# Performance work log

Measured on AMD Instinct MI355X. Metric: run time of the kernel, lower is better.

The kernel has to match this reference:

```python
import jax, jax.numpy as jnp
import numpy as np

B, S, IN_DIM, D_MODEL, NUM_HEADS = 4, 2048, 1024, 1024, 16
HEAD_DIM = D_MODEL // NUM_HEADS
CAUSAL = True
NEG = -9000000000000000.0


def _xavier(key, shape):
    fan_out, fan_in = shape
    limit = (6.0 / (fan_in + fan_out)) ** 0.5
    return jax.random.uniform(key, shape, jnp.float32, -limit, limit)


def setup_inputs() -> dict:
    key = jax.random.key(0)
    ks = jax.random.split(key, 5)
    x = jax.random.normal(ks[0], (B, S, IN_DIM), jnp.float32)
    Wq = _xavier(ks[1], (D_MODEL, IN_DIM))
    Wk = _xavier(ks[2], (D_MODEL, IN_DIM))
    Wv = _xavier(ks[3], (D_MODEL, IN_DIM))
    Wo = _xavier(ks[4], (D_MODEL, D_MODEL))
    bq = jnp.zeros((D_MODEL,), jnp.float32)
    bk = jnp.zeros((D_MODEL,), jnp.float32)
    bv = jnp.zeros((D_MODEL,), jnp.float32)
    bo = jnp.zeros((D_MODEL,), jnp.float32)
    return {"x": x, "Wq": Wq, "bq": bq, "Wk": Wk, "bk": bk,
            "Wv": Wv, "bv": bv, "Wo": Wo, "bo": bo}


def reference(x, Wq, bq, Wk, bk, Wv, bv, Wo, bo):
    batch, seq, _ = x.shape
    # torch Linear: y = x @ W.T + b
    q = x @ Wq.T + bq
    k = x @ Wk.T + bk
    v = x @ Wv.T + bv
    # [B, S, H, Dh] -> [B, H, S, Dh]
    def split(t):
        return t.reshape(batch, seq, NUM_HEADS, HEAD_DIM).transpose(0, 2, 1, 3)
    q, k, v = split(q), split(k), split(v)
    scores = jnp.einsum('bhqd,bhkd->bhqk', q, k) / jnp.sqrt(jnp.float32(HEAD_DIM))
    if CAUSAL:
        mask = jnp.tril(jnp.ones((seq, seq), bool))
        scores = jnp.where(mask, scores, jnp.float32(NEG))
    attn = jax.nn.softmax(scores, axis=-1)
    out = jnp.einsum('bhqk,bhkd->bhqd', attn, v)
    out = out.transpose(0, 2, 1, 3).reshape(batch, seq, D_MODEL)
    return out @ Wo.T + bo
```

## Files before the change

kernel.cpp:

```cpp
#include <hip/hip_runtime.h>
#include <cstdint>
#include <cmath>

typedef unsigned short u16;
typedef __attribute__((ext_vector_type(4))) float f32x4;
typedef __attribute__((ext_vector_type(8))) short bf16x8;

#define D_MODEL 1024
#define SEQ     2048
#define BATCH   4
#define NHEAD   16
#define MTOT    (BATCH*SEQ)
#define NXE     ((size_t)MTOT * D_MODEL)

static_assert(sizeof(bf16x8) == 16, "frag size");

__device__ __forceinline__ float bf2f(u16 u) {
    union { uint32_t i; float f; } v; v.i = ((uint32_t)u) << 16; return v.f;
}
__device__ __forceinline__ u16 f2bf(float x) {
    union { float f; uint32_t i; } v; v.f = x;
    uint32_t r = (v.i + 0x7FFFu + ((v.i >> 16) & 1u)) >> 16;
    return (u16)r;
}
__device__ __forceinline__ u16 f2bf_trunc(float x) {
    union { float f; uint32_t i; } v; v.f = x;
    return (u16)(v.i >> 16);
}

#if defined(__has_builtin)
#if __has_builtin(__builtin_amdgcn_exp2f)
#define EXP2_FAST(x) __builtin_amdgcn_exp2f(x)
#endif
#endif
#ifndef EXP2_FAST
#define EXP2_FAST(x) exp2f(x)
#endif

typedef const __attribute__((address_space(1))) void* gptr_t;
typedef __attribute__((address_space(3))) void* sptr_t;
__device__ __forceinline__ void gload_lds16(const void* g, void* l) {
    __builtin_amdgcn_global_load_lds((gptr_t)g, (sptr_t)l, 16, 0, 0);
}

__device__ __forceinline__ u16 u4get(const uint4& v, int e) {
    const uint32_t w = ((e >> 1) == 0) ? v.x : ((e >> 1) == 1) ? v.y
                     : ((e >> 1) == 2) ? v.z : v.w;
    return (u16)((e & 1) ? (w >> 16) : (w & 0xFFFFu));
}

__global__ __launch_bounds__(256) void diag_write(float* __restrict__ out, float v) {
    size_t i = (size_t)blockIdx.x * 256 + threadIdx.x;
    for (; i < NXE; i += (size_t)gridDim.x * 256) out[i] = v;
}

__global__ void detect_dtype(const u16* __restrict__ x, int* __restrict__ flag) {
    __shared__ int cnt;
    if (threadIdx.x == 0) cnt = 0;
    __syncthreads();
    int c = 0;
#pragma unroll
    for (int k = 0; k < 16; ++k) {
        u16 e = x[2 * (threadIdx.x * 16 + k)];
        int ex = (e >> 7) & 0xFF;
        if (e == 0 || (ex >= 100 && ex <= 140)) ++c;
    }
    atomicAdd(&cnt, c);
    __syncthreads();
    if (threadIdx.x == 0) *flag = (cnt >= 3500) ? 1 : 0;
}

struct CvtArgs { const void* src[9]; u16* dst[9]; int n[9]; };

__global__ __launch_bounds__(256) void cvt_all(CvtArgs a, const int* __restrict__ flag) {
    const int seg = blockIdx.y;
    const int n = a.n[seg];
    const int i = (blockIdx.x * 256 + threadIdx.x) * 8;
    if (i >= n) return;
    u16* d = a.dst[seg] + i;
    if (*flag) {
        *(uint4*)d = *(const uint4*)((const u16*)a.src[seg] + i);
    } else {
        const float* s = (const float*)a.src[seg] + i;
        u16 tmp[8];
#pragma unroll
        for (int k = 0; k < 8; ++k) tmp[k] = f2bf(s[k]);
        *(uint4*)d = *(uint4*)tmp;
    }
}

template <typename OutT>
__device__ __forceinline__ void gemm_body(
    const u16* __restrict__ A, const u16* __restrict__ W,
    const u16* __restrict__ bias, OutT* __restrict__ C,
    int M, int N, int K)
{
    __shared__ __align__(16) u16 As[128 * 32];
    __shared__ __align__(16) u16 Bs[128 * 32];

    const int t    = threadIdx.x;
    const int wave = t >> 6;
    const int ln   = t & 15;
    const int qd   = (t >> 4) & 3;
    const int m0   = blockIdx.x * 128;
    const int n0   = blockIdx.y * 128;
    const int wm   = (wave >> 1) * 64;
    const int wn   = (wave & 1) * 64;

    const int srow = t >> 2;
    const int scol = (t & 3) * 8;
    const u16* gA = A + (size_t)(m0 + srow) * K + scol;
    const u16* gB = W + (size_t)(n0 + srow) * K + scol;
    u16* lA = &As[wave * 512];
    u16* lB = &Bs[wave * 512];

    f32x4 acc[4][4] = {};

    for (int k0 = 0; k0 < K; k0 += 32) {
        __syncthreads();
        gload_lds16(gA + k0,                   lA);
        gload_lds16(gA + (size_t)64 * K + k0,  lA + 2048);
        gload_lds16(gB + k0,                   lB);
        gload_lds16(gB + (size_t)64 * K + k0,  lB + 2048);
        __syncthreads();

        bf16x8 af[4], bfr[4];
#pragma unroll
        for (int i = 0; i < 4; ++i)
            af[i] = *(const bf16x8*)&As[(wm + i * 16 + ln) * 32 + qd * 8];
#pragma unroll
        for (int j = 0; j < 4; ++j)
            bfr[j] = *(const bf16x8*)&Bs[(wn + j * 16 + ln) * 32 + qd * 8];
#pragma unroll
        for (int i = 0; i < 4; ++i)
#pragma unroll
            for (int j = 0; j < 4; ++j)
                acc[i][j] = __builtin_amdgcn_mfma_f32_16x16x32_bf16(
                    af[i], bfr[j], acc[i][j], 0, 0, 0);
    }

    float bv[4];
#pragma unroll
    for (int j = 0; j < 4; ++j) bv[j] = bf2f(bias[n0 + wn + j * 16 + ln]);

#pragma unroll
    for (int i = 0; i < 4; ++i)
#pragma unroll
        for (int r = 0; r < 4; ++r) {
            int row = m0 + wm + i * 16 + qd * 4 + r;
            OutT* crow = C + (size_t)row * N + n0 + wn + ln;
#pragma unroll
            for (int j = 0; j < 4; ++j) {
                float v = acc[i][j][r] + bv[j];
                if constexpr (sizeof(OutT) == 2) crow[j * 16] = f2bf(v);
                else                             crow[j * 16] = v;
            }
        }
}

__global__ __launch_bounds__(256) void gemm_qkv(
    const u16* __restrict__ A,
    const u16* __restrict__ W0, const u16* __restrict__ W1, const u16* __restrict__ W2,
    const u16* __restrict__ b0, const u16* __restrict__ b1, const u16* __restrict__ b2,
    u16* __restrict__ C0, u16* __restrict__ C1, u16* __restrict__ C2,
    int M, int N, int K)
{
    const u16* W; const u16* bias; u16* C;
    if (blockIdx.z == 0)      { W = W0; bias = b0; C = C0; }
    else if (blockIdx.z == 1) { W = W1; bias = b1; C = C1; }
    else                      { W = W2; bias = b2; C = C2; }
    gemm_body<u16>(A, W, bias, C, M, N, K);
}

__global__ __launch_bounds__(256) void gemm_final_f32(
    const u16* __restrict__ A, const u16* __restrict__ W,
    const u16* __restrict__ bias, float* __restrict__ C, int M, int N, int K)
{
    gemm_body<float>(A, W, bias, C, M, N, K);
}

__global__ __launch_bounds__(256) void transpose_v(
    const u16* __restrict__ V, u16* __restrict__ VT)
{
    __shared__ u16 T[64][72];
    const int st = blockIdx.x;
    const int bh = blockIdx.y;
    const int b  = bh >> 4;
    const int h  = bh & 15;
    const int t  = threadIdx.x;

    const int sr = t >> 2;
    const int dc = (t & 3) * 16;
    const u16* src = V + ((size_t)b * SEQ + st * 64 + sr) * D_MODEL + h * 64 + dc;
    const uint4 a0 = *(const uint4*)src;
    const uint4 a1 = *(const uint4*)(src + 8);
#pragma unroll
    for (int e = 0; e < 8; ++e) T[dc + e][sr]     = u4get(a0, e);
#pragma unroll
    for (int e = 0; e < 8; ++e) T[dc + 8 + e][sr] = u4get(a1, e);
    __syncthreads();

    const int d  = t >> 2;
    const int sc = (t & 3) * 16;
    u16* dst = VT + ((size_t)bh * 64 + d) * SEQ + st * 64 + sc;
    *(uint4*)dst       = *(const uint4*)&T[d][sc];
    *(uint4*)(dst + 8) = *(const uint4*)&T[d][sc + 8];
}

__global__ __launch_bounds__(64) void flash_attn(
    const u16* __restrict__ Qg, const u16* __restrict__ Kg,
    const u16* __restrict__ VTg, u16* __restrict__ Og)
{
    __shared__ __align__(16) u16 Vsh[64 * 64];
    __shared__ __align__(16) u16 Psh[32 * 64];

    const int lane = threadIdx.x;
    const int ln   = lane & 15;
    const int qd   = lane >> 4;
    const int psw  = (ln & 7) << 3;

    const int bh = blockIdx.y;
    const int qw = (63 - (int)blockIdx.x + bh) & 63;
    const int b  = bh >> 4;
    const int h  = bh & 15;
    const int h0 = h * 64;
    const size_t rowBase = (size_t)b * SEQ * D_MODEL;
    const int qw0 = qw * 32;
    const int ktMax = qw >> 1;

    const int vdG = lane >> 3;
    const int vsw = ((lane & 7) * 8) ^ (vdG << 3);
    const u16* vtRow0 = VTg + ((size_t)(bh * 64 + vdG)) * SEQ + vsw;

    const float SCL = 0.18033688011112042f;

    bf16x8 qf[2][2];
#pragma unroll
    for (int i = 0; i < 2; ++i)
#pragma unroll
        for (int ks = 0; ks < 2; ++ks)
            qf[i][ks] = *(const bf16x8*)(Qg + rowBase
                + (size_t)(qw0 + i * 16 + ln) * D_MODEL + h0 + ks * 32 + qd * 8);

    float m_run[2], l_run[2];
#pragma unroll
    for (int i = 0; i < 2; ++i) { m_run[i] = -30000.0f; l_run[i] = 0.f; }
    f32x4 oacc[2][4] = {};

    for (int kt = 0; kt <= ktMax; ++kt) {
        __syncthreads();
        {
            const u16* vbase = vtRow0 + kt * 64;
#pragma unroll
            for (int p = 0; p < 8; ++p)
                gload_lds16(vbase + (size_t)(p * 8) * SEQ, &Vsh[p * 512]);
        }

        f32x4 sacc[4][2] = {};
#pragma unroll
        for (int ks = 0; ks < 2; ++ks) {
            bf16x8 kf[4];
#pragma unroll
            for (int j = 0; j < 4; ++j)
                kf[j] = *(const bf16x8*)(Kg + rowBase
                    + (size_t)(kt * 64 + j * 16 + ln) * D_MODEL + h0 + ks * 32 + qd * 8);
            __builtin_amdgcn_s_setprio(1);
#pragma unroll
            for (int j = 0; j < 4; ++j)
#pragma unroll
                for (int i = 0; i < 2; ++i)
                    sacc[j][i] = __builtin_amdgcn_mfma_f32_16x16x32_bf16(
                        kf[j], qf[i][ks], sacc[j][i], 0, 0, 0);
            __builtin_amdgcn_s_setprio(0);
        }

        if (kt == ktMax) {
#pragma unroll
            for (int j = 0; j < 4; ++j)
#pragma unroll
                for (int r = 0; r < 4; ++r) {
                    const int kpos = kt * 64 + j * 16 + qd * 4 + r;
#pragma unroll
                    for (int i = 0; i < 2; ++i) {
                        const int qpos = qw0 + i * 16 + ln;
                        float s = sacc[j][i][r] * SCL;
                        sacc[j][i][r] = (kpos > qpos) ? -30000.0f : s;
                    }
                }
        } else {
#pragma unroll
            for (int j = 0; j < 4; ++j)
#pragma unroll
                for (int i = 0; i < 2; ++i)
#pragma unroll
                    for (int r = 0; r < 4; ++r)
                        sacc[j][i][r] *= SCL;
        }

        float mx[2];
#pragma unroll
        for (int i = 0; i < 2; ++i) {
            float m0 = sacc[0][i][0];
#pragma unroll
            for (int j = 0; j < 4; ++j)
#pragma unroll
                for (int r = 0; r < 4; ++r) m0 = fmaxf(m0, sacc[j][i][r]);
            m0 = fmaxf(m0, __shfl_xor(m0, 16));
            m0 = fmaxf(m0, __shfl_xor(m0, 32));
            mx[i] = m0;
        }

        const bool grow = !(__all((mx[0] <= m_run[0] + 8.f) &&
                                  (mx[1] <= m_run[1] + 8.f)));
        if (grow) {
#pragma unroll
            for (int i = 0; i < 2; ++i) {
                const float mo = m_run[i];
                const float mn = fmaxf(mo, mx[i]);
                const float alpha = EXP2_FAST(mo - mn);
                m_run[i] = mn;
                l_run[i] *= alpha;
#pragma unroll
                for (int r = 0; r < 4; ++r) {
                    const float ar = __shfl(alpha, qd * 4 + r);
#pragma unroll
                    for (int j = 0; j < 4; ++j) oacc[i][j][r] *= ar;
                }
            }
        }

#pragma unroll
        for (int i = 0; i < 2; ++i) {
            const float mn = m_run[i];
            float rs = 0.f;
#pragma unroll
            for (int j = 0; j < 4; ++j) {
                u16 tp[4];
#pragma unroll
                for (int r = 0; r < 4; ++r) {
                    float p = EXP2_FAST(sacc[j][i][r] - mn);
                    rs += p;
                    tp[r] = f2bf_trunc(p);
                }
                uint2 w;
                w.x = (uint32_t)tp[0] | ((uint32_t)tp[1] << 16);
                w.y = (uint32_t)tp[2] | ((uint32_t)tp[3] << 16);
                *(uint2*)&Psh[(i * 16 + ln) * 64 + ((j * 16 + qd * 4) ^ psw)] = w;
            }
            rs += __shfl_xor(rs, 16);
            rs += __shfl_xor(rs, 32);
            l_run[i] += rs;
        }

        __syncthreads();

#pragma unroll
        for (int ks = 0; ks < 2; ++ks) {
            bf16x8 pa[2];
#pragma unroll
            for (int i = 0; i < 2; ++i)
                pa[i] = *(const bf16x8*)&Psh[(i * 16 + ln) * 64
                                             + ((ks * 32 + qd * 8) ^ psw)];
            __builtin_amdgcn_s_setprio(1);
#pragma unroll
            for (int j = 0; j < 4; ++j) {
                const int d = j * 16 + ln;
                const bf16x8 vb = *(const bf16x8*)&Vsh[d * 64
                    + ((ks * 32 + qd * 8) ^ ((ln & 7) << 3))];
#pragma unroll
                for (int i = 0; i < 2; ++i)
                    oacc[i][j] = __builtin_amdgcn_mfma_f32_16x16x32_bf16(
                        pa[i], vb, oacc[i][j], 0, 0, 0);
            }
            __builtin_amdgcn_s_setprio(0);
        }
    }

#pragma unroll
    for (int i = 0; i < 2; ++i)
#pragma unroll
        for (int r = 0; r < 4; ++r) {
            const float lr = __shfl(l_run[i], qd * 4 + r);
            const float inv = 1.f / lr;
            const int qrow = qw0 + i * 16 + qd * 4 + r;
            u16* orow = Og + rowBase + (size_t)qrow * D_MODEL + h0 + ln;
#pragma unroll
            for (int j = 0; j < 4; ++j)
                orow[j * 16] = f2bf(oacc[i][j][r] * inv);
        }
}

static inline bool ranges_overlap(const void* a, size_t an, const void* b, size_t bn) {
    uintptr_t x0 = (uintptr_t)a, x1 = x0 + an;
    uintptr_t y0 = (uintptr_t)b, y1 = y0 + bn;
    return x0 < y1 && y0 < x1;
}

extern "C" void kernel_launch(void* const* d_in, const int* in_sizes, int n_in,
                              void* d_out, int out_size, void* d_ws, size_t ws_size,
                              hipStream_t stream)
{
    int e = 0;
    const int expect[9] = { 8388608, 1048576, 1024, 1048576, 1024,
                            1048576, 1024, 1048576, 1024 };
    if (n_in != 9) e = 59;
    if (!e) for (int i = 0; i < 9; ++i)
        if (in_sizes[i] != expect[i]) { e = 60 + i; break; }
    if (!e && out_size != (int)NXE) e = 53;
    if (!e && ranges_overlap(d_ws, ws_size, d_out, (size_t)out_size * 4)) e = 55;

    const size_t NX = NXE;
    const size_t NW = (size_t)D_MODEL * D_MODEL;
    const size_t NB = D_MODEL;

    const size_t need = (64 + 4 * NW + 4 * NB + 2 * NX) * 2;
    if (!e && ws_size < need) e = 50;
    if (e) { diag_write<<<2048, 256, 0, stream>>>((float*)d_out, ldexpf(1.0f, e)); return; }

    u16* ws   = (u16*)d_ws;
    int* flag = (int*)ws;
    u16* Wqb  = ws + 64;
    u16* Wkb  = Wqb + NW;
    u16* Wvb  = Wkb + NW;
    u16* Wob  = Wvb + NW;
    u16* bqb  = Wob + NW;
    u16* bkb  = bqb + NB;
    u16* bvb  = bkb + NB;
    u16* bob  = bvb + NB;
    u16* Kw   = bob + NB;
    u16* Vw   = Kw  + NX;

    u16* xb  = (u16*)d_out;
    u16* Qw  = xb + NX;
    u16* VTw = xb;
    u16* Ow  = Vw;

    detect_dtype<<<1, 256, 0, stream>>>((const u16*)d_in[0], flag);

    CvtArgs ca;
    const void* srcs[9] = { d_in[0], d_in[1], d_in[3], d_in[5], d_in[7],
                            d_in[2], d_in[4], d_in[6], d_in[8] };
    u16* dsts[9] = { xb, Wqb, Wkb, Wvb, Wob, bqb, bkb, bvb, bob };
    int  ns[9]   = { (int)NX, (int)NW, (int)NW, (int)NW, (int)NW,
                     (int)NB, (int)NB, (int)NB, (int)NB };
    for (int i = 0; i < 9; ++i) { ca.src[i] = srcs[i]; ca.dst[i] = dsts[i]; ca.n[i] = ns[i]; }
    cvt_all<<<dim3((unsigned)((NX + 2047) / 2048), 9), 256, 0, stream>>>(ca, flag);

    gemm_qkv<<<dim3(MTOT / 128, D_MODEL / 128, 3), 256, 0, stream>>>(
        xb, Wqb, Wkb, Wvb, bqb, bkb, bvb, Qw, Kw, Vw, MTOT, D_MODEL, D_MODEL);

    transpose_v<<<dim3(SEQ / 64, BATCH * NHEAD), 256, 0, stream>>>(Vw, VTw);

    flash_attn<<<dim3(SEQ / 32, BATCH * NHEAD), 64, 0, stream>>>(Qw, Kw, VTw, Ow);

    gemm_final_f32<<<dim3(MTOT / 128, D_MODEL / 128), 256, 0, stream>>>(
        Ow, Wob, bob, (float*)d_out, MTOT, D_MODEL, D_MODEL);
}
```

Baseline: 334.2 us.

## Split flash-attention KV loop across two waves with final softmax merge

Each block now runs two waves that handle alternating key tiles for the same 32 query rows. Each wave keeps its own V and P shared-memory buffers, and the per-iteration __syncthreads become per-wave waitcnt fences. At the end, wave 1 writes its running max, sum and output accumulator to shared memory, and wave 0 merges the two partial softmax states before writing the output. This roughly halves the serial KV-loop length per block, which targets the long causal rows, at the cost of more shared memory, a merge step and one more block-wide barrier.

Result: no change. 332.9 us (-0.4%).

```diff
diff --git a/kernel.cpp b/kernel.cpp
--- a/kernel.cpp
+++ b/kernel.cpp
@@ -207,14 +207,15 @@
     *(uint4*)(dst + 8) = *(const uint4*)&T[d][sc + 8];
 }
 
-__global__ __launch_bounds__(64) void flash_attn(
+__global__ __launch_bounds__(128) void flash_attn(
     const u16* __restrict__ Qg, const u16* __restrict__ Kg,
     const u16* __restrict__ VTg, u16* __restrict__ Og)
 {
-    __shared__ __align__(16) u16 Vsh[64 * 64];
-    __shared__ __align__(16) u16 Psh[32 * 64];
-
-    const int lane = threadIdx.x;
+    __shared__ __align__(16) u16 Vsh[2][64 * 64];
+    __shared__ __align__(16) u16 Psh[2][32 * 64];
+
+    const int wv   = threadIdx.x >> 6;
+    const int lane = threadIdx.x & 63;
     const int ln   = lane & 15;
     const int qd   = lane >> 4;
     const int psw  = (ln & 7) << 3;
@@ -228,6 +229,9 @@
     const int qw0 = qw * 32;
     const int ktMax = qw >> 1;
 
+    u16* VshW = &Vsh[wv][0];
+    u16* P    = &Psh[wv][0];
+
     const int vdG = lane >> 3;
     const int vsw = ((lane & 7) * 8) ^ (vdG << 3);
     const u16* vtRow0 = VTg + ((size_t)(bh * 64 + vdG)) * SEQ + vsw;
@@ -247,13 +251,15 @@
     for (int i = 0; i < 2; ++i) { m_run[i] = -30000.0f; l_run[i] = 0.f; }
     f32x4 oacc[2][4] = {};
 
-    for (int kt = 0; kt <= ktMax; ++kt) {
-        __syncthreads();
+    for (int kt = wv; kt <= ktMax; kt += 2) {
+        asm volatile("s_waitcnt lgkmcnt(0)" ::: "memory");
+        __builtin_amdgcn_sched_barrier(0);
+
         {
             const u16* vbase = vtRow0 + kt * 64;
 #pragma unroll
             for (int p = 0; p < 8; ++p)
-                gload_lds16(vbase + (size_t)(p * 8) * SEQ, &Vsh[p * 512]);
+                gload_lds16(vbase + (size_t)(p * 8) * SEQ, &VshW[p * 512]);
         }
 
         f32x4 sacc[4][2] = {};
@@ -345,27 +351,28 @@
                 uint2 w;
                 w.x = (uint32_t)tp[0] | ((uint32_t)tp[1] << 16);
                 w.y = (uint32_t)tp[2] | ((uint32_t)tp[3] << 16);
-                *(uint2*)&Psh[(i * 16 + ln) * 64 + ((j * 16 + qd * 4) ^ psw)] = w;
+                *(uint2*)&P[(i * 16 + ln) * 64 + ((j * 16 + qd * 4) ^ psw)] = w;
             }
             rs += __shfl_xor(rs, 16);
             rs += __shfl_xor(rs, 32);
             l_run[i] += rs;
         }
 
-        __syncthreads();
+        asm volatile("s_waitcnt vmcnt(0)" ::: "memory");
+        __builtin_amdgcn_sched_barrier(0);
 
 #pragma unroll
         for (int ks = 0; ks < 2; ++ks) {
             bf16x8 pa[2];
 #pragma unroll
             for (int i = 0; i < 2; ++i)
-                pa[i] = *(const bf16x8*)&Psh[(i * 16 + ln) * 64
-                                             + ((ks * 32 + qd * 8) ^ psw)];
+                pa[i] = *(const bf16x8*)&P[(i * 16 + ln) * 64
+                                           + ((ks * 32 + qd * 8) ^ psw)];
             __builtin_amdgcn_s_setprio(1);
 #pragma unroll
             for (int j = 0; j < 4; ++j) {
                 const int d = j * 16 + ln;
-                const bf16x8 vb = *(const bf16x8*)&Vsh[d * 64
+                const bf16x8 vb = *(const bf16x8*)&VshW[d * 64
                     + ((ks * 32 + qd * 8) ^ ((ln & 7) << 3))];
 #pragma unroll
                 for (int i = 0; i < 2; ++i)
@@ -376,18 +383,47 @@
         }
     }
 
-#pragma unroll
-    for (int i = 0; i < 2; ++i)
-#pragma unroll
-        for (int r = 0; r < 4; ++r) {
-            const float lr = __shfl(l_run[i], qd * 4 + r);
-            const float inv = 1.f / lr;
-            const int qrow = qw0 + i * 16 + qd * 4 + r;
-            u16* orow = Og + rowBase + (size_t)qrow * D_MODEL + h0 + ln;
-#pragma unroll
-            for (int j = 0; j < 4; ++j)
-                orow[j * 16] = f2bf(oacc[i][j][r] * inv);
-        }
+    float* exO  = (float*)&Vsh[1][0];
+    float* exML = (float*)&Psh[1][0];
+    if (wv == 1) {
+        if (qd == 0) {
+#pragma unroll
+            for (int i = 0; i < 2; ++i) {
+                exML[i * 16 + ln]      = m_run[i];
+                exML[32 + i * 16 + ln] = l_run[i];
+            }
+        }
+#pragma unroll
+        for (int i = 0; i < 2; ++i)
+#pragma unroll
+            for (int j = 0; j < 4; ++j)
+#pragma unroll
+                for (int r = 0; r < 4; ++r)
+                    exO[(i * 16 + qd * 4 + r) * 64 + j * 16 + ln] = oacc[i][j][r];
+    }
+    __syncthreads();
+    if (wv == 0) {
+#pragma unroll
+        for (int i = 0; i < 2; ++i)
+#pragma unroll
+            for (int r = 0; r < 4; ++r) {
+                const int row = i * 16 + qd * 4 + r;
+                const float m0r = __shfl(m_run[i], qd * 4 + r);
+                const float l0r = __shfl(l_run[i], qd * 4 + r);
+                const float m1r = exML[row];
+                const float l1r = exML[32 + row];
+                const float mm  = fmaxf(m0r, m1r);
+                const float a0  = EXP2_FAST(m0r - mm);
+                const float a1  = EXP2_FAST(m1r - mm);
+                const float inv = 1.f / (a0 * l0r + a1 * l1r);
+                const int qrow = qw0 + row;
+                u16* orow = Og + rowBase + (size_t)qrow * D_MODEL + h0 + ln;
+#pragma unroll
+                for (int j = 0; j < 4; ++j)
+                    orow[j * 16] = f2bf((a0 * oacc[i][j][r]
+                                         + a1 * exO[row * 64 + j * 16 + ln]) * inv);
+            }
+    }
 }
 
 static inline bool ranges_overlap(const void* a, size_t an, const void* b, size_t bn) {
@@ -451,7 +487,7 @@
 
     transpose_v<<<dim3(SEQ / 64, BATCH * NHEAD), 256, 0, stream>>>(Vw, VTw);
 
-    flash_attn<<<dim3(SEQ / 32, BATCH * NHEAD), 64, 0, stream>>>(Qw, Kw, VTw, Ow);
+    flash_attn<<<dim3(SEQ / 32, BATCH * NHEAD), 128, 0, stream>>>(Qw, Kw, VTw, Ow);
 
     gemm_final_f32<<<dim3(MTOT / 128, D_MODEL / 128), 256, 0, stream>>>(
         Ow, Wob, bob, (float*)d_out, MTOT, D_MODEL, D_MODEL);
```
